# Performance work log

Measured on AMD Instinct MI355X. Metric: run time of the kernel, lower is better.

## Reference

```python
import jax, jax.numpy as jnp
import numpy as np

VAR0, VAR1 = 0.1, 0.2          # SSD encode variances
POS_T, NEG_T, NPR = 0.5, 0.4, 3  # pos/neg thresholds, negpos_ratio
BBOX_ALPHA, CONF_ALPHA = 1.5, 1.0


def point_form(b):
    # cxcywh -> x1y1x2y2
    return jnp.concatenate([b[..., :2] - b[..., 2:] / 2, b[..., :2] + b[..., 2:] / 2], -1)


def jaccard(a, b):
    # a:[n,4], b:[m,4] in xyxy -> IoU [n,m]
    tl = jnp.maximum(a[:, None, :2], b[None, :, :2])
    br = jnp.minimum(a[:, None, 2:], b[None, :, 2:])
    inter = jnp.prod(jnp.clip(br - tl, 0.0), -1)
    area_a = jnp.prod(a[:, 2:] - a[:, :2], -1)[:, None]
    area_b = jnp.prod(b[:, 2:] - b[:, :2], -1)[None, :]
    return inter / jnp.clip(area_a + area_b - inter, 1e-10)


def encode(matched, priors):
    # matched: xyxy GT per prior; priors: cxcywh
    g_c = ((matched[:, :2] + matched[:, 2:]) / 2 - priors[:, :2]) / (VAR0 * priors[:, 2:])
    g_wh = jnp.log(jnp.clip((matched[:, 2:] - matched[:, :2]) / priors[:, 2:], 1e-8)) / VAR1
    return jnp.concatenate([g_c, g_wh], -1)


def match_one(gt_box, gt_lab, priors):
    # gt_box:[G,4] xyxy, gt_lab:[G], priors:[P,4] cxcywh
    ov = jaccard(gt_box, point_form(priors))            # [G,P]
    bt_over = ov.max(0)                                  # best GT overlap per prior [P]
    bt_idx = ov.argmax(0)                                # [P]
    bp_idx = ov.argmax(1)                                # best prior per GT [G]
    G = gt_box.shape[0]
    bt_over = bt_over.at[bp_idx].set(2.0)                # force-match best priors
    bt_idx = bt_idx.at[bp_idx].set(jnp.arange(G))
    matched = gt_box[bt_idx]                             # [P,4]
    conf_t = gt_lab[bt_idx]
    conf_t = jnp.where(bt_over < POS_T, jnp.where(bt_over < NEG_T, 0, -1), conf_t)
    return encode(matched, priors), conf_t


def reference(loc_data, conf_data, priors, gt_bboxes, gt_labels):
    B, P, C = conf_data.shape
    loc_t, conf_t = jax.vmap(match_one)(gt_bboxes, gt_labels, priors)
    loc_t = jax.lax.stop_gradient(loc_t)                 # targets are detached in torch
    pos = conf_t > 0                                     # [B,P]
    num_pos = pos.sum(-1)                                # [B]
    dt = loc_data.dtype
    pos_w = pos.astype(dt) / jnp.clip(num_pos, 1).astype(dt)[:, None]

    # localization: per-image-normalized smooth L1 over positives
    d = loc_data - loc_t
    sl1 = jnp.where(jnp.abs(d) < 1.0, 0.5 * d * d, jnp.abs(d) - 0.5)
    loss_B = (pos_w[:, :, None] * sl1).sum() * BBOX_ALPHA

    # OHEM confidence loss: mine top negpos_ratio*num_pos hardest negatives per image
    loss_c = jax.nn.logsumexp(conf_data, -1) - conf_data[..., 0]
    loss_c = jnp.where(pos | (conf_t < 0), 0.0, jax.lax.stop_gradient(loss_c))
    rank = jnp.argsort(jnp.argsort(-loss_c, -1), -1)     # descending rank [B,P]
    num_neg = jnp.clip(NPR * num_pos, 0, P - 1)
    neg = (rank < num_neg[:, None]) & (conf_t == 0)
    keep = (pos | neg).astype(dt)
    logp = jax.nn.log_softmax(conf_data, -1)
    tgt = jnp.clip(conf_t, 0)
    ce = -jnp.take_along_axis(logp, tgt[..., None], -1)[..., 0]
    loss_C = (keep * ce).sum() * CONF_ALPHA

    return jnp.stack([loss_B, loss_C]) / B               # [2]: (loss_B, loss_C)


def setup_inputs() -> dict:
    key = jax.random.key(0)
    k = jax.random.split(key, 8)
    B, P, C, G = 16, 19248, 81, 16
    loc_data = jax.random.normal(k[0], (B, P, 4), jnp.float32)
    conf_data = jax.random.normal(k[1], (B, P, C), jnp.float32)
    pc = jax.random.uniform(k[2], (B, P, 2)) * 0.9 + 0.05
    pwh = jax.random.uniform(k[3], (B, P, 2)) * 0.25 + 0.05
    priors = jnp.concatenate([pc, pwh], -1).astype(jnp.float32)  # cxcywh
    gc = jax.random.uniform(k[4], (B, G, 2)) * 0.8 + 0.1
    gwh = jax.random.uniform(k[5], (B, G, 2)) * 0.3 + 0.05
    gt_bboxes = jnp.clip(point_form(jnp.concatenate([gc, gwh], -1)), 0.0, 1.0).astype(jnp.float32)
    gt_labels = jax.random.randint(k[6], (B, G), 1, C)
    return {"loc_data": loc_data, "conf_data": conf_data, "priors": priors,
            "gt_bboxes": gt_bboxes, "gt_labels": gt_labels}
```

## Files before the change

kernel.cpp:

```cpp
#include <hip/hip_runtime.h>
#include <math.h>

#define NB 16
#define NP 19248
#define NC 81
#define NG 16
#define NBC 301
#define NWPB (NBC * 4)

static __device__ __forceinline__ float smoothl1(float d) {
    float a = fabsf(d);
    return (a < 1.f) ? 0.5f * d * d : (a - 0.5f);
}

static __device__ __forceinline__ unsigned long long umax64(unsigned long long a, unsigned long long b) {
    return a > b ? a : b;
}

__global__ void __launch_bounds__(256, 6) k_main(
        const float* __restrict__ conf,
        const float* __restrict__ loc,
        const float* __restrict__ priors,
        const float* __restrict__ gtb,
        const int* __restrict__ gtl,
        unsigned long long* __restrict__ kws,
        float* __restrict__ mlc,
        int* __restrict__ pnp, float* __restrict__ psl, float* __restrict__ pce,
        float* __restrict__ out) {
    __shared__ float sc[4][1296];
    const int b = blockIdx.y;
    const int tid = threadIdx.x;
    if (b == 0 && blockIdx.x == 0 && tid < 2) out[tid] = 0.f;
    const int w = tid >> 6, lane = tid & 63;
    const int rb = blockIdx.x * 64 + w * 16;
    const bool wvalid = rb < NP;
    const int rb_c = wvalid ? rb : (NP - 16);

    const float4* src = (const float4*)(conf + ((size_t)b * NP + rb_c) * 81);
    float4* dst = (float4*)sc[w];
    #pragma unroll
    for (int i = 0; i < 5; ++i) dst[lane + 64 * i] = src[lane + 64 * i];
    if (lane < 4) dst[lane + 320] = src[lane + 320];

    const int r = lane >> 2, c = lane & 3;
    const int p = rb_c + r;
    const int bp = b * NP + p;
    const int wslot = blockIdx.x * 4 + w;

    const float4 prr = *(const float4*)(priors + (size_t)bp * 4);
    const float px1 = prr.x - prr.z * 0.5f, py1 = prr.y - prr.w * 0.5f;
    const float px2 = prr.x + prr.z * 0.5f, py2 = prr.y + prr.w * 0.5f;
    const float areaP = (px2 - px1) * (py2 - py1);
    const unsigned int pk = 0xFFFFFFFFu - (unsigned int)p;
    unsigned long long kq = 0ULL;
    #pragma unroll
    for (int j = 0; j < 4; ++j) {
        const int g = c * 4 + j;
        const float4 gb = *(const float4*)(gtb + (size_t)(b * NG + g) * 4);
        float iw = fminf(gb.z, px2) - fmaxf(gb.x, px1);
        float ih = fminf(gb.w, py2) - fmaxf(gb.y, py1);
        float inter = fmaxf(iw, 0.f) * fmaxf(ih, 0.f);
        float areaG = (gb.z - gb.x) * (gb.w - gb.y);
        float ov = inter / fmaxf(areaG + areaP - inter, 1e-10f);
        const unsigned long long ub = (unsigned long long)__float_as_uint(ov) << 32;
        kq = umax64(kq, ub | (unsigned long long)(15 - g));
        unsigned long long kg = ub | (unsigned long long)pk;
        #pragma unroll
        for (int off = 4; off <= 32; off <<= 1)
            kg = umax64(kg, (unsigned long long)__shfl_xor((unsigned long long)kg, off));
        if (lane < 4)
            kws[((size_t)(b * NG) + lane * 4 + j) * NWPB + wslot] = kg;
    }
    kq = umax64(kq, (unsigned long long)__shfl_xor((unsigned long long)kq, 1, 4));
    kq = umax64(kq, (unsigned long long)__shfl_xor((unsigned long long)kq, 2, 4));
    const float over = __uint_as_float((unsigned int)(kq >> 32));
    const int bi = 15 - (int)(kq & 0xFULL);

    int ct;
    if (over < 0.4f) ct = 0;
    else if (over < 0.5f) ct = -1;
    else ct = gtl[b * NG + bi];
    if (!wvalid) ct = 0;
    const int tgt = ct > 0 ? ct : 0;

    __builtin_amdgcn_wave_barrier();

    const float* row = sc[w] + r * 81;
    float s = 0.f, ctg = 0.f;
    #pragma unroll
    for (int k = 0; k < 21; ++k) {
        int cc = c + 4 * k;
        if (cc < 81) {
            float v = row[cc];
            s += __expf(v);
            ctg += (cc == tgt) ? v : 0.f;
        }
    }
    s += __shfl_xor(s, 1, 4);   s += __shfl_xor(s, 2, 4);
    ctg += __shfl_xor(ctg, 1, 4); ctg += __shfl_xor(ctg, 2, 4);
    const float c0 = row[0];
    const float lse = __logf(s);

    if (c == 0 && wvalid) mlc[bp] = (ct == 0) ? (lse - c0) : -1.0f;

    float vsl = 0.f, vce = 0.f; int vnp = 0;
    if (c == 0 && ct > 0) {
        const float4 gb = *(const float4*)(gtb + (size_t)(b * NG + bi) * 4);
        float lt0 = ((gb.x + gb.z) * 0.5f - prr.x) / (0.1f * prr.z);
        float lt1 = ((gb.y + gb.w) * 0.5f - prr.y) / (0.1f * prr.w);
        float lt2 = logf(fmaxf((gb.z - gb.x) / prr.z, 1e-8f)) / 0.2f;
        float lt3 = logf(fmaxf((gb.w - gb.y) / prr.w, 1e-8f)) / 0.2f;
        const float4 l4 = *(const float4*)(loc + (size_t)bp * 4);
        vsl = smoothl1(l4.x - lt0) + smoothl1(l4.y - lt1) +
              smoothl1(l4.z - lt2) + smoothl1(l4.w - lt3);
        vce = lse - ctg;
        vnp = 1;
    }
    #pragma unroll
    for (int o = 32; o >= 1; o >>= 1) {
        vnp += __shfl_xor(vnp, o);
        vsl += __shfl_xor(vsl, o);
        vce += __shfl_xor(vce, o);
    }
    if (lane == 0) {
        const int idx = b * NWPB + wslot;
        pnp[idx] = vnp; psl[idx] = vsl; pce[idx] = vce;
    }
}

__global__ void __launch_bounds__(1024) k_finish(
        const float* __restrict__ conf,
        const float* __restrict__ loc,
        const float* __restrict__ priors,
        const float* __restrict__ gtb,
        const int* __restrict__ gtl,
        const unsigned long long* __restrict__ kws,
        const float* __restrict__ mlc,
        const int* __restrict__ pnp,
        const float* __restrict__ psl,
        const float* __restrict__ pce,
        float* __restrict__ out) {
    const int b = blockIdx.x, tid = threadIdx.x;
    __shared__ unsigned int hist[4096];
    __shared__ unsigned long long list[1024];
    __shared__ unsigned int s_jstar, s_need, s_cnt;
    __shared__ unsigned long long s_thr;
    __shared__ unsigned int wtot[16], wsuf[16];
    __shared__ float wsum[16];
    __shared__ int wnp[16]; __shared__ float wsl[16], wcp[16];
    __shared__ int s_np; __shared__ float s_sl, s_cp;
    __shared__ unsigned int fprior[16];
    __shared__ unsigned int zap[16];
    __shared__ int s_dnp; __shared__ float s_dsl, s_dce;

    const float4* v4 = (const float4*)(mlc + (size_t)b * NP);
    float4 rv[5];
    #pragma unroll
    for (int j = 0; j < 5; ++j) {
        int i = tid + 1024 * j;
        rv[j] = (i < NP / 4) ? v4[i] : make_float4(-1.f, -1.f, -1.f, -1.f);
    }

    {
        int np_ = 0; float sl_ = 0.f, cp_ = 0.f;
        for (int i = tid; i < NWPB; i += 1024) {
            np_ += pnp[b * NWPB + i];
            sl_ += psl[b * NWPB + i];
            cp_ += pce[b * NWPB + i];
        }
        #pragma unroll
        for (int o = 32; o >= 1; o >>= 1) {
            np_ += __shfl_xor(np_, o);
            sl_ += __shfl_xor(sl_, o);
            cp_ += __shfl_xor(cp_, o);
        }
        if ((tid & 63) == 0) { wnp[tid >> 6] = np_; wsl[tid >> 6] = sl_; wcp[tid >> 6] = cp_; }
    }
    {
        const int wv = tid >> 6, lane = tid & 63;
        unsigned long long kk = 0ULL;
        const unsigned long long* kp = kws + ((size_t)(b * NG) + wv) * NWPB;
        for (int i = lane; i < NWPB; i += 64) kk = umax64(kk, kp[i]);
        #pragma unroll
        for (int o = 32; o >= 1; o >>= 1)
            kk = umax64(kk, (unsigned long long)__shfl_xor((unsigned long long)kk, o));
        if (lane == 0) fprior[wv] = 0xFFFFFFFFu - (unsigned int)(kk & 0xFFFFFFFFULL);
    }
    if (tid == 0) { s_cnt = 0u; s_thr = ~0ULL; s_dnp = 0; s_dsl = 0.f; s_dce = 0.f; }
    for (int i = tid; i < 4096; i += 1024) hist[i] = 0u;
    __syncthreads();

    if (tid < 64) {
        const int g = tid >> 2, c = tid & 3;
        const unsigned int pstar = fprior[g];
        bool winner = true;
        for (int g2 = g + 1; g2 < NG; ++g2) if (fprior[g2] == pstar) winner = false;
        int old_ct = 1;
        if (winner) {
            const int pp = (int)pstar;
            const int bpp = b * NP + pp;
            const float4 prr = *(const float4*)(priors + (size_t)bpp * 4);
            const float px1 = prr.x - prr.z * 0.5f, py1 = prr.y - prr.w * 0.5f;
            const float px2 = prr.x + prr.z * 0.5f, py2 = prr.y + prr.w * 0.5f;
            const float areaP = (px2 - px1) * (py2 - py1);
            unsigned long long kq = 0ULL;
            #pragma unroll
            for (int j = 0; j < 4; ++j) {
                const int g2 = c * 4 + j;
                const float4 gb = *(const float4*)(gtb + (size_t)(b * NG + g2) * 4);
                float iw = fminf(gb.z, px2) - fmaxf(gb.x, px1);
                float ih = fminf(gb.w, py2) - fmaxf(gb.y, py1);
                float inter = fmaxf(iw, 0.f) * fmaxf(ih, 0.f);
                float areaG = (gb.z - gb.x) * (gb.w - gb.y);
                float ov = inter / fmaxf(areaG + areaP - inter, 1e-10f);
                kq = umax64(kq, ((unsigned long long)__float_as_uint(ov) << 32) |
                                (unsigned long long)(15 - g2));
            }
            kq = umax64(kq, (unsigned long long)__shfl_xor((unsigned long long)kq, 1, 4));
            kq = umax64(kq, (unsigned long long)__shfl_xor((unsigned long long)kq, 2, 4));
            const float over = __uint_as_float((unsigned int)(kq >> 32));
            const int obi = 15 - (int)(kq & 0xFULL);
            if (over < 0.4f) old_ct = 0;
            else if (over < 0.5f) old_ct = -1;
            else old_ct = gtl[b * NG + obi];
            const int new_lab = gtl[b * NG + g];
            const int old_tgt = old_ct > 0 ? old_ct : 0;
            const float* row = conf + (size_t)bpp * 81;
            float s = 0.f, vnew = 0.f, vold = 0.f;
            #pragma unroll
            for (int k = 0; k < 21; ++k) {
                int cc = c + 4 * k;
                if (cc < 81) {
                    float v = row[cc];
                    s += __expf(v);
                    vnew += (cc == new_lab) ? v : 0.f;
                    vold += (cc == old_tgt) ? v : 0.f;
                }
            }
            s += __shfl_xor(s, 1, 4);       s += __shfl_xor(s, 2, 4);
            vnew += __shfl_xor(vnew, 1, 4); vnew += __shfl_xor(vnew, 2, 4);
            vold += __shfl_xor(vold, 1, 4); vold += __shfl_xor(vold, 2, 4);
            if (c == 0) {
                const float lse = __logf(s);
                float dce = (old_ct > 0) ? (vold - vnew) : (lse - vnew);
                const float4 gb = *(const float4*)(gtb + (size_t)(b * NG + g) * 4);
                float lt0 = ((gb.x + gb.z) * 0.5f - prr.x) / (0.1f * prr.z);
                float lt1 = ((gb.y + gb.w) * 0.5f - prr.y) / (0.1f * prr.w);
                float lt2 = logf(fmaxf((gb.z - gb.x) / prr.z, 1e-8f)) / 0.2f;
                float lt3 = logf(fmaxf((gb.w - gb.y) / prr.w, 1e-8f)) / 0.2f;
                const float4 l4 = *(const float4*)(loc + (size_t)bpp * 4);
                float dsl = smoothl1(l4.x - lt0) + smoothl1(l4.y - lt1) +
                            smoothl1(l4.z - lt2) + smoothl1(l4.w - lt3);
                if (old_ct > 0) {
                    const float4 go = *(const float4*)(gtb + (size_t)(b * NG + obi) * 4);
                    float ot0 = ((go.x + go.z) * 0.5f - prr.x) / (0.1f * prr.z);
                    float ot1 = ((go.y + go.w) * 0.5f - prr.y) / (0.1f * prr.w);
                    float ot2 = logf(fmaxf((go.z - go.x) / prr.z, 1e-8f)) / 0.2f;
                    float ot3 = logf(fmaxf((go.w - go.y) / prr.w, 1e-8f)) / 0.2f;
                    dsl -= smoothl1(l4.x - ot0) + smoothl1(l4.y - ot1) +
                           smoothl1(l4.z - ot2) + smoothl1(l4.w - ot3);
                }
                if (old_ct <= 0) atomicAdd(&s_dnp, 1);
                atomicAdd(&s_dsl, dsl);
                atomicAdd(&s_dce, dce);
            }
        }
        if (c == 0) zap[g] = (winner && old_ct == 0) ? pstar : 0xFFFFFFFFu;
    }
    __syncthreads();

    #pragma unroll
    for (int z = 0; z < NG; ++z) {
        unsigned int u = zap[z];
        if (u != 0xFFFFFFFFu) {
            unsigned int q = u >> 2, cc = u & 3u;
            if ((int)(q & 1023u) == tid) {
                unsigned int jj = q >> 10;
                #pragma unroll
                for (int j = 0; j < 5; ++j) if ((unsigned int)j == jj) {
                    if (cc == 0) rv[j].x = -1.f;
                    else if (cc == 1) rv[j].y = -1.f;
                    else if (cc == 2) rv[j].z = -1.f;
                    else rv[j].w = -1.f;
                }
            }
        }
    }
    if (tid == 0) {
        int np_ = s_dnp; float sl_ = s_dsl, cp_ = s_dce;
        #pragma unroll
        for (int i = 0; i < 16; ++i) { np_ += wnp[i]; sl_ += wsl[i]; cp_ += wcp[i]; }
        s_np = np_; s_sl = sl_; s_cp = cp_;
    }
    #pragma unroll
    for (int j = 0; j < 5; ++j) {
        float vv[4] = {rv[j].x, rv[j].y, rv[j].z, rv[j].w};
        #pragma unroll
        for (int cth = 0; cth < 4; ++cth)
            if (vv[cth] >= 0.f)
                atomicAdd(&hist[min((unsigned int)(vv[cth] * 256.f), 4095u)], 1u);
    }
    __syncthreads();
    const int np = s_np;
    const unsigned int k = (unsigned int)min(3 * np, NP - 1);

    if (k > 0) {
        unsigned int c0 = hist[tid * 4], c1 = hist[tid * 4 + 1],
                     c2 = hist[tid * 4 + 2], c3 = hist[tid * 4 + 3];
        unsigned int t2 = c2 + c3, t1 = c1 + t2, t0 = c0 + t1;
        unsigned int s = t0;
        const int lane = tid & 63, w = tid >> 6;
        #pragma unroll
        for (int o = 1; o < 64; o <<= 1) {
            unsigned int vv = __shfl_down(s, o);
            if (lane + o < 64) s += vv;
        }
        if (lane == 0) wtot[w] = s;
        __syncthreads();
        if (tid < 16) {
            unsigned int acc = 0;
            for (int j = tid + 1; j < 16; ++j) acc += wtot[j];
            wsuf[tid] = acc;
        }
        __syncthreads();
        const unsigned int base = wsuf[w] + (s - t0);
        unsigned int b0 = base + t0, b1 = base + t1, b2 = base + t2, b3 = base + c3;
        hist[tid * 4] = b0; hist[tid * 4 + 1] = b1;
        hist[tid * 4 + 2] = b2; hist[tid * 4 + 3] = b3;
        __syncthreads();
        const unsigned int total = hist[0];
        if (k >= total) {
            if (tid == 0) s_thr = 0ULL;
        } else {
            unsigned int n3 = (tid * 4 + 4 < 4096) ? hist[tid * 4 + 4] : 0u;
            if (b0 >= k && b1 < k) { s_jstar = tid * 4;     s_need = k - b1; }
            if (b1 >= k && b2 < k) { s_jstar = tid * 4 + 1; s_need = k - b2; }
            if (b2 >= k && b3 < k) { s_jstar = tid * 4 + 2; s_need = k - b3; }
            if (b3 >= k && n3 < k) { s_jstar = tid * 4 + 3; s_need = k - n3; }
            __syncthreads();
            const unsigned int jstar = s_jstar, need = s_need;
            #pragma unroll
            for (int j = 0; j < 5; ++j) {
                float vv[4] = {rv[j].x, rv[j].y, rv[j].z, rv[j].w};
                #pragma unroll
                for (int cth = 0; cth < 4; ++cth) {
                    if (vv[cth] >= 0.f &&
                        min((unsigned int)(vv[cth] * 256.f), 4095u) == jstar) {
                        unsigned int pos = atomicAdd(&s_cnt, 1u);
                        if (pos < 1024u) {
                            int pidx = 4 * (tid + 1024 * j) + cth;
                            list[pos] = ((unsigned long long)__float_as_uint(vv[cth]) << 32) |
                                        (unsigned long long)(0xFFFFFFFFu - (unsigned int)pidx);
                        }
                    }
                }
            }
            __syncthreads();
            const unsigned int cnt = s_cnt;
            if (cnt <= 1024u) {
                if (tid < (int)cnt) {
                    unsigned long long me = list[tid];
                    unsigned int rk = 0;
                    for (unsigned int j = 0; j < cnt; ++j) rk += (list[j] > me) ? 1u : 0u;
                    if (rk == need - 1) s_thr = me;
                }
            } else if (tid == 0) {
                s_thr = ((unsigned long long)__float_as_uint((float)jstar / 256.f)) << 32;
            }
        }
    }
    __syncthreads();
    const unsigned long long thr = s_thr;

    float sum = 0.f;
    #pragma unroll
    for (int j = 0; j < 5; ++j) {
        float vv[4] = {rv[j].x, rv[j].y, rv[j].z, rv[j].w};
        #pragma unroll
        for (int cth = 0; cth < 4; ++cth) {
            if (vv[cth] >= 0.f) {
                int pidx = 4 * (tid + 1024 * j) + cth;
                unsigned long long key = ((unsigned long long)__float_as_uint(vv[cth]) << 32) |
                                         (unsigned long long)(0xFFFFFFFFu - (unsigned int)pidx);
                if (key >= thr) sum += vv[cth];
            }
        }
    }
    #pragma unroll
    for (int o = 32; o >= 1; o >>= 1) sum += __shfl_xor(sum, o);
    if ((tid & 63) == 0) wsum[tid >> 6] = sum;
    __syncthreads();
    if (tid == 0) {
        float neg = 0.f;
        #pragma unroll
        for (int i = 0; i < 16; ++i) neg += wsum[i];
        float lb = s_sl / (float)max(np, 1);
        float lc = s_cp + neg;
        atomicAdd(&out[0], lb * 1.5f / (float)NB);
        atomicAdd(&out[1], lc / (float)NB);
    }
}

extern "C" void kernel_launch(void* const* d_in, const int* in_sizes, int n_in,
                              void* d_out, int out_size, void* d_ws, size_t ws_size,
                              hipStream_t stream) {
    const float* loc    = (const float*)d_in[0];
    const float* conf   = (const float*)d_in[1];
    const float* priors = (const float*)d_in[2];
    const float* gtb    = (const float*)d_in[3];
    const int*   gtl    = (const int*)d_in[4];
    float* out = (float*)d_out;

    char* w = (char*)d_ws;
    const size_t KWS = (size_t)NB * NG * NWPB * 8;
    const size_t P1  = (size_t)NB * NWPB * 4;
    unsigned long long* kws = (unsigned long long*)w;
    int*   pnp = (int*)  (w + KWS);
    float* psl = (float*)(w + KWS + P1);
    float* pce = (float*)(w + KWS + 2 * P1);
    float* mlc = (float*)(w + KWS + 3 * P1);

    k_main<<<dim3(NBC, NB), 256, 0, stream>>>(conf, loc, priors, gtb, gtl,
                                              kws, mlc, pnp, psl, pce, out);
    k_finish<<<NB, 1024, 0, stream>>>(conf, loc, priors, gtb, gtl,
                                      kws, mlc, pnp, psl, pce, out);
}
```

Before: 186.1 us.

## Fuse finish kernel into main kernel via last-block-per-image completion counter

Merges the two kernels into one. The last block to finish for each image, found with an atomic counter and thread fences, runs the matching fix-up, the histogram and the hard-negative top-k selection with 256 threads instead of a separate 1024-thread launch. A second counter lets the last image write the final outputs directly instead of using atomics, and a memset resets the counters each call. The aim is to remove a kernel launch and its gap and to overlap the per-image tail with other images still in progress. In exchange the tail runs with 4x fewer threads, rereads the mining values from global memory three times, and adds a memset launch.

```diff
diff --git a/kernel.cpp b/kernel.cpp
--- a/kernel.cpp
+++ b/kernel.cpp
@@ -7,6 +7,7 @@
 #define NG 16
 #define NBC 301
 #define NWPB (NBC * 4)
+#define NV4 (NP / 4)
 
 static __device__ __forceinline__ float smoothl1(float d) {
     float a = fabsf(d);
@@ -17,27 +18,29 @@
     return a > b ? a : b;
 }
 
-__global__ void __launch_bounds__(256, 6) k_main(
+__global__ void __launch_bounds__(256, 6) k_all(
         const float* __restrict__ conf,
         const float* __restrict__ loc,
         const float* __restrict__ priors,
         const float* __restrict__ gtb,
         const int* __restrict__ gtl,
+        unsigned int* __restrict__ cnt,
         unsigned long long* __restrict__ kws,
         float* __restrict__ mlc,
         int* __restrict__ pnp, float* __restrict__ psl, float* __restrict__ pce,
+        int* __restrict__ rnp, float* __restrict__ rsl, float* __restrict__ rlc,
         float* __restrict__ out) {
-    __shared__ float sc[4][1296];
+    __shared__ unsigned long long smem[3072];
+    float* sc = (float*)smem;
     const int b = blockIdx.y;
     const int tid = threadIdx.x;
-    if (b == 0 && blockIdx.x == 0 && tid < 2) out[tid] = 0.f;
     const int w = tid >> 6, lane = tid & 63;
     const int rb = blockIdx.x * 64 + w * 16;
     const bool wvalid = rb < NP;
     const int rb_c = wvalid ? rb : (NP - 16);
 
     const float4* src = (const float4*)(conf + ((size_t)b * NP + rb_c) * 81);
-    float4* dst = (float4*)sc[w];
+    float4* dst = (float4*)(sc + w * 1296);
     #pragma unroll
     for (int i = 0; i < 5; ++i) dst[lane + 64 * i] = src[lane + 64 * i];
     if (lane < 4) dst[lane + 320] = src[lane + 320];
@@ -85,7 +88,7 @@
 
     __builtin_amdgcn_wave_barrier();
 
-    const float* row = sc[w] + r * 81;
+    const float* row = sc + w * 1296 + r * 81;
     float s = 0.f, ctg = 0.f;
     #pragma unroll
     for (int k = 0; k < 21; ++k) {
@@ -126,44 +129,28 @@
         const int idx = b * NWPB + wslot;
         pnp[idx] = vnp; psl[idx] = vsl; pce[idx] = vce;
     }
-}
-
-__global__ void __launch_bounds__(1024) k_finish(
-        const float* __restrict__ conf,
-        const float* __restrict__ loc,
-        const float* __restrict__ priors,
-        const float* __restrict__ gtb,
-        const int* __restrict__ gtl,
-        const unsigned long long* __restrict__ kws,
-        const float* __restrict__ mlc,
-        const int* __restrict__ pnp,
-        const float* __restrict__ psl,
-        const float* __restrict__ pce,
-        float* __restrict__ out) {
-    const int b = blockIdx.x, tid = threadIdx.x;
-    __shared__ unsigned int hist[4096];
-    __shared__ unsigned long long list[1024];
-    __shared__ unsigned int s_jstar, s_need, s_cnt;
+
+    __shared__ int s_last;
+    __threadfence();
+    if (tid == 0) s_last = (atomicAdd(&cnt[b], 1u) == NBC - 1) ? 1 : 0;
+    __syncthreads();
+    if (!s_last) return;
+    __threadfence();
+
+    unsigned int* hist = (unsigned int*)smem;
+    unsigned long long* list = smem + 2048;
+    __shared__ unsigned int s_jstar, s_need, s_cnt, s_total;
     __shared__ unsigned long long s_thr;
-    __shared__ unsigned int wtot[16], wsuf[16];
-    __shared__ float wsum[16];
-    __shared__ int wnp[16]; __shared__ float wsl[16], wcp[16];
+    __shared__ int wnp4[4]; __shared__ float wsl4[4], wcp4[4];
+    __shared__ unsigned int wtot4[4], wsuf4[4];
+    __shared__ float wsum4[4];
     __shared__ int s_np; __shared__ float s_sl, s_cp;
-    __shared__ unsigned int fprior[16];
-    __shared__ unsigned int zap[16];
+    __shared__ unsigned int fprior[16], zap[16];
     __shared__ int s_dnp; __shared__ float s_dsl, s_dce;
-
-    const float4* v4 = (const float4*)(mlc + (size_t)b * NP);
-    float4 rv[5];
-    #pragma unroll
-    for (int j = 0; j < 5; ++j) {
-        int i = tid + 1024 * j;
-        rv[j] = (i < NP / 4) ? v4[i] : make_float4(-1.f, -1.f, -1.f, -1.f);
-    }
 
     {
         int np_ = 0; float sl_ = 0.f, cp_ = 0.f;
-        for (int i = tid; i < NWPB; i += 1024) {
+        for (int i = tid; i < NWPB; i += 256) {
             np_ += pnp[b * NWPB + i];
             sl_ += psl[b * NWPB + i];
             cp_ += pce[b * NWPB + i];
@@ -174,89 +161,88 @@
             sl_ += __shfl_xor(sl_, o);
             cp_ += __shfl_xor(cp_, o);
         }
-        if ((tid & 63) == 0) { wnp[tid >> 6] = np_; wsl[tid >> 6] = sl_; wcp[tid >> 6] = cp_; }
-    }
-    {
-        const int wv = tid >> 6, lane = tid & 63;
+        if (lane == 0) { wnp4[w] = np_; wsl4[w] = sl_; wcp4[w] = cp_; }
+    }
+    for (int q = 0; q < 4; ++q) {
+        const int g = w * 4 + q;
         unsigned long long kk = 0ULL;
-        const unsigned long long* kp = kws + ((size_t)(b * NG) + wv) * NWPB;
+        const unsigned long long* kp = kws + ((size_t)(b * NG) + g) * NWPB;
         for (int i = lane; i < NWPB; i += 64) kk = umax64(kk, kp[i]);
         #pragma unroll
         for (int o = 32; o >= 1; o >>= 1)
             kk = umax64(kk, (unsigned long long)__shfl_xor((unsigned long long)kk, o));
-        if (lane == 0) fprior[wv] = 0xFFFFFFFFu - (unsigned int)(kk & 0xFFFFFFFFULL);
+        if (lane == 0) fprior[g] = 0xFFFFFFFFu - (unsigned int)(kk & 0xFFFFFFFFULL);
     }
     if (tid == 0) { s_cnt = 0u; s_thr = ~0ULL; s_dnp = 0; s_dsl = 0.f; s_dce = 0.f; }
-    for (int i = tid; i < 4096; i += 1024) hist[i] = 0u;
     __syncthreads();
 
     if (tid < 64) {
-        const int g = tid >> 2, c = tid & 3;
-        const unsigned int pstar = fprior[g];
+        const int fg = tid >> 2, fc = tid & 3;
+        const unsigned int pstar = fprior[fg];
         bool winner = true;
-        for (int g2 = g + 1; g2 < NG; ++g2) if (fprior[g2] == pstar) winner = false;
+        for (int g2 = fg + 1; g2 < NG; ++g2) if (fprior[g2] == pstar) winner = false;
         int old_ct = 1;
         if (winner) {
             const int pp = (int)pstar;
             const int bpp = b * NP + pp;
-            const float4 prr = *(const float4*)(priors + (size_t)bpp * 4);
-            const float px1 = prr.x - prr.z * 0.5f, py1 = prr.y - prr.w * 0.5f;
-            const float px2 = prr.x + prr.z * 0.5f, py2 = prr.y + prr.w * 0.5f;
-            const float areaP = (px2 - px1) * (py2 - py1);
-            unsigned long long kq = 0ULL;
+            const float4 fpr = *(const float4*)(priors + (size_t)bpp * 4);
+            const float fx1 = fpr.x - fpr.z * 0.5f, fy1 = fpr.y - fpr.w * 0.5f;
+            const float fx2 = fpr.x + fpr.z * 0.5f, fy2 = fpr.y + fpr.w * 0.5f;
+            const float fareaP = (fx2 - fx1) * (fy2 - fy1);
+            unsigned long long kq2 = 0ULL;
             #pragma unroll
             for (int j = 0; j < 4; ++j) {
-                const int g2 = c * 4 + j;
+                const int g2 = fc * 4 + j;
                 const float4 gb = *(const float4*)(gtb + (size_t)(b * NG + g2) * 4);
-                float iw = fminf(gb.z, px2) - fmaxf(gb.x, px1);
-                float ih = fminf(gb.w, py2) - fmaxf(gb.y, py1);
+                float iw = fminf(gb.z, fx2) - fmaxf(gb.x, fx1);
+                float ih = fminf(gb.w, fy2) - fmaxf(gb.y, fy1);
                 float inter = fmaxf(iw, 0.f) * fmaxf(ih, 0.f);
                 float areaG = (gb.z - gb.x) * (gb.w - gb.y);
-                float ov = inter / fmaxf(areaG + areaP - inter, 1e-10f);
-                kq = umax64(kq, ((unsigned long long)__float_as_uint(ov) << 32) |
-                                (unsigned long long)(15 - g2));
-            }
-            kq = umax64(kq, (unsigned long long)__shfl_xor((unsigned long long)kq, 1, 4));
-            kq = umax64(kq, (unsigned long long)__shfl_xor((unsigned long long)kq, 2, 4));
-            const float over = __uint_as_float((unsigned int)(kq >> 32));
-            const int obi = 15 - (int)(kq & 0xFULL);
-            if (over < 0.4f) old_ct = 0;
-            else if (over < 0.5f) old_ct = -1;
+                float ov = inter / fmaxf(areaG + fareaP - inter, 1e-10f);
+                kq2 = umax64(kq2, ((unsigned long long)__float_as_uint(ov) << 32) |
+                                  (unsigned long long)(15 - g2));
+            }
+            kq2 = umax64(kq2, (unsigned long long)__shfl_xor((unsigned long long)kq2, 1, 4));
+            kq2 = umax64(kq2, (unsigned long long)__shfl_xor((unsigned long long)kq2, 2, 4));
+            const float fover = __uint_as_float((unsigned int)(kq2 >> 32));
+            const int obi = 15 - (int)(kq2 & 0xFULL);
+            if (fover < 0.4f) old_ct = 0;
+            else if (fover < 0.5f) old_ct = -1;
             else old_ct = gtl[b * NG + obi];
-            const int new_lab = gtl[b * NG + g];
+            const int new_lab = gtl[b * NG + fg];
             const int old_tgt = old_ct > 0 ? old_ct : 0;
-            const float* row = conf + (size_t)bpp * 81;
-            float s = 0.f, vnew = 0.f, vold = 0.f;
+            const float* frow = conf + (size_t)bpp * 81;
+            float fs = 0.f, vnew = 0.f, vold = 0.f;
             #pragma unroll
             for (int k = 0; k < 21; ++k) {
-                int cc = c + 4 * k;
+                int cc = fc + 4 * k;
                 if (cc < 81) {
-                    float v = row[cc];
-                    s += __expf(v);
+                    float v = frow[cc];
+                    fs += __expf(v);
                     vnew += (cc == new_lab) ? v : 0.f;
                     vold += (cc == old_tgt) ? v : 0.f;
                 }
             }
-            s += __shfl_xor(s, 1, 4);       s += __shfl_xor(s, 2, 4);
+            fs += __shfl_xor(fs, 1, 4);     fs += __shfl_xor(fs, 2, 4);
             vnew += __shfl_xor(vnew, 1, 4); vnew += __shfl_xor(vnew, 2, 4);
             vold += __shfl_xor(vold, 1, 4); vold += __shfl_xor(vold, 2, 4);
-            if (c == 0) {
-                const float lse = __logf(s);
-                float dce = (old_ct > 0) ? (vold - vnew) : (lse - vnew);
-                const float4 gb = *(const float4*)(gtb + (size_t)(b * NG + g) * 4);
-                float lt0 = ((gb.x + gb.z) * 0.5f - prr.x) / (0.1f * prr.z);
-                float lt1 = ((gb.y + gb.w) * 0.5f - prr.y) / (0.1f * prr.w);
-                float lt2 = logf(fmaxf((gb.z - gb.x) / prr.z, 1e-8f)) / 0.2f;
-                float lt3 = logf(fmaxf((gb.w - gb.y) / prr.w, 1e-8f)) / 0.2f;
+            if (fc == 0) {
+                const float flse = __logf(fs);
+                float dce = (old_ct > 0) ? (vold - vnew) : (flse - vnew);
+                const float4 gb = *(const float4*)(gtb + (size_t)(b * NG + fg) * 4);
+                float lt0 = ((gb.x + gb.z) * 0.5f - fpr.x) / (0.1f * fpr.z);
+                float lt1 = ((gb.y + gb.w) * 0.5f - fpr.y) / (0.1f * fpr.w);
+                float lt2 = logf(fmaxf((gb.z - gb.x) / fpr.z, 1e-8f)) / 0.2f;
+                float lt3 = logf(fmaxf((gb.w - gb.y) / fpr.w, 1e-8f)) / 0.2f;
                 const float4 l4 = *(const float4*)(loc + (size_t)bpp * 4);
                 float dsl = smoothl1(l4.x - lt0) + smoothl1(l4.y - lt1) +
                             smoothl1(l4.z - lt2) + smoothl1(l4.w - lt3);
                 if (old_ct > 0) {
                     const float4 go = *(const float4*)(gtb + (size_t)(b * NG + obi) * 4);
-                    float ot0 = ((go.x + go.z) * 0.5f - prr.x) / (0.1f * prr.z);
-                    float ot1 = ((go.y + go.w) * 0.5f - prr.y) / (0.1f * prr.w);
-                    float ot2 = logf(fmaxf((go.z - go.x) / prr.z, 1e-8f)) / 0.2f;
-                    float ot3 = logf(fmaxf((go.w - go.y) / prr.w, 1e-8f)) / 0.2f;
+                    float ot0 = ((go.x + go.z) * 0.5f - fpr.x) / (0.1f * fpr.z);
+                    float ot1 = ((go.y + go.w) * 0.5f - fpr.y) / (0.1f * fpr.w);
+                    float ot2 = logf(fmaxf((go.z - go.x) / fpr.z, 1e-8f)) / 0.2f;
+                    float ot3 = logf(fmaxf((go.w - go.y) / fpr.w, 1e-8f)) / 0.2f;
                     dsl -= smoothl1(l4.x - ot0) + smoothl1(l4.y - ot1) +
                            smoothl1(l4.z - ot2) + smoothl1(l4.w - ot3);
                 }
@@ -265,90 +251,77 @@
                 atomicAdd(&s_dce, dce);
             }
         }
-        if (c == 0) zap[g] = (winner && old_ct == 0) ? pstar : 0xFFFFFFFFu;
-    }
-    __syncthreads();
-
-    #pragma unroll
-    for (int z = 0; z < NG; ++z) {
-        unsigned int u = zap[z];
-        if (u != 0xFFFFFFFFu) {
-            unsigned int q = u >> 2, cc = u & 3u;
-            if ((int)(q & 1023u) == tid) {
-                unsigned int jj = q >> 10;
-                #pragma unroll
-                for (int j = 0; j < 5; ++j) if ((unsigned int)j == jj) {
-                    if (cc == 0) rv[j].x = -1.f;
-                    else if (cc == 1) rv[j].y = -1.f;
-                    else if (cc == 2) rv[j].z = -1.f;
-                    else rv[j].w = -1.f;
-                }
-            }
-        }
-    }
+        if (fc == 0) zap[fg] = (winner && old_ct == 0) ? pstar : 0xFFFFFFFFu;
+    }
+    __syncthreads();
+
+    if (tid < NG) {
+        unsigned int u = zap[tid];
+        if (u != 0xFFFFFFFFu) mlc[(size_t)b * NP + u] = -1.0f;
+    }
+    __threadfence_block();
     if (tid == 0) {
         int np_ = s_dnp; float sl_ = s_dsl, cp_ = s_dce;
         #pragma unroll
-        for (int i = 0; i < 16; ++i) { np_ += wnp[i]; sl_ += wsl[i]; cp_ += wcp[i]; }
+        for (int i = 0; i < 4; ++i) { np_ += wnp4[i]; sl_ += wsl4[i]; cp_ += wcp4[i]; }
         s_np = np_; s_sl = sl_; s_cp = cp_;
     }
-    #pragma unroll
-    for (int j = 0; j < 5; ++j) {
-        float vv[4] = {rv[j].x, rv[j].y, rv[j].z, rv[j].w};
-        #pragma unroll
-        for (int cth = 0; cth < 4; ++cth)
-            if (vv[cth] >= 0.f)
-                atomicAdd(&hist[min((unsigned int)(vv[cth] * 256.f), 4095u)], 1u);
+    for (int i = tid; i < 4096; i += 256) hist[i] = 0u;
+    __syncthreads();
+
+    const float4* mv4 = (const float4*)(mlc + (size_t)b * NP);
+    for (int i = tid; i < NV4; i += 256) {
+        float4 v = mv4[i];
+        if (v.x >= 0.f) atomicAdd(&hist[min((unsigned int)(v.x * 256.f), 4095u)], 1u);
+        if (v.y >= 0.f) atomicAdd(&hist[min((unsigned int)(v.y * 256.f), 4095u)], 1u);
+        if (v.z >= 0.f) atomicAdd(&hist[min((unsigned int)(v.z * 256.f), 4095u)], 1u);
+        if (v.w >= 0.f) atomicAdd(&hist[min((unsigned int)(v.w * 256.f), 4095u)], 1u);
     }
     __syncthreads();
     const int np = s_np;
     const unsigned int k = (unsigned int)min(3 * np, NP - 1);
 
     if (k > 0) {
-        unsigned int c0 = hist[tid * 4], c1 = hist[tid * 4 + 1],
-                     c2 = hist[tid * 4 + 2], c3 = hist[tid * 4 + 3];
-        unsigned int t2 = c2 + c3, t1 = c1 + t2, t0 = c0 + t1;
-        unsigned int s = t0;
-        const int lane = tid & 63, w = tid >> 6;
+        unsigned int ttot = 0;
+        for (int i = 0; i < 16; ++i) ttot += hist[tid * 16 + i];
+        unsigned int s2 = ttot;
         #pragma unroll
         for (int o = 1; o < 64; o <<= 1) {
-            unsigned int vv = __shfl_down(s, o);
-            if (lane + o < 64) s += vv;
-        }
-        if (lane == 0) wtot[w] = s;
+            unsigned int vv = __shfl_down(s2, o);
+            if (lane + o < 64) s2 += vv;
+        }
+        if (lane == 0) wtot4[w] = s2;
         __syncthreads();
-        if (tid < 16) {
-            unsigned int acc = 0;
-            for (int j = tid + 1; j < 16; ++j) acc += wtot[j];
-            wsuf[tid] = acc;
+        if (tid < 4) {
+            unsigned int a = 0;
+            for (int j = tid + 1; j < 4; ++j) a += wtot4[j];
+            wsuf4[tid] = a;
         }
         __syncthreads();
-        const unsigned int base = wsuf[w] + (s - t0);
-        unsigned int b0 = base + t0, b1 = base + t1, b2 = base + t2, b3 = base + c3;
-        hist[tid * 4] = b0; hist[tid * 4 + 1] = b1;
-        hist[tid * 4 + 2] = b2; hist[tid * 4 + 3] = b3;
+        const unsigned int base = wsuf4[w] + (s2 - ttot);
+        if (tid == 0) s_total = base + ttot;
+        unsigned int run = 0;
+        for (int i = 15; i >= 0; --i) {
+            unsigned int Sj1 = base + run;
+            run += hist[tid * 16 + i];
+            unsigned int Sj = base + run;
+            if (Sj >= k && Sj1 < k) { s_jstar = tid * 16 + i; s_need = k - Sj1; }
+        }
         __syncthreads();
-        const unsigned int total = hist[0];
-        if (k >= total) {
+        if (k >= s_total) {
             if (tid == 0) s_thr = 0ULL;
         } else {
-            unsigned int n3 = (tid * 4 + 4 < 4096) ? hist[tid * 4 + 4] : 0u;
-            if (b0 >= k && b1 < k) { s_jstar = tid * 4;     s_need = k - b1; }
-            if (b1 >= k && b2 < k) { s_jstar = tid * 4 + 1; s_need = k - b2; }
-            if (b2 >= k && b3 < k) { s_jstar = tid * 4 + 2; s_need = k - b3; }
-            if (b3 >= k && n3 < k) { s_jstar = tid * 4 + 3; s_need = k - n3; }
-            __syncthreads();
             const unsigned int jstar = s_jstar, need = s_need;
-            #pragma unroll
-            for (int j = 0; j < 5; ++j) {
-                float vv[4] = {rv[j].x, rv[j].y, rv[j].z, rv[j].w};
+            for (int i = tid; i < NV4; i += 256) {
+                float4 v = mv4[i];
+                float vv[4] = {v.x, v.y, v.z, v.w};
                 #pragma unroll
                 for (int cth = 0; cth < 4; ++cth) {
                     if (vv[cth] >= 0.f &&
                         min((unsigned int)(vv[cth] * 256.f), 4095u) == jstar) {
                         unsigned int pos = atomicAdd(&s_cnt, 1u);
                         if (pos < 1024u) {
-                            int pidx = 4 * (tid + 1024 * j) + cth;
+                            int pidx = 4 * i + cth;
                             list[pos] = ((unsigned long long)__float_as_uint(vv[cth]) << 32) |
                                         (unsigned long long)(0xFFFFFFFFu - (unsigned int)pidx);
                         }
@@ -356,12 +329,12 @@
                 }
             }
             __syncthreads();
-            const unsigned int cnt = s_cnt;
-            if (cnt <= 1024u) {
-                if (tid < (int)cnt) {
-                    unsigned long long me = list[tid];
+            const unsigned int cc2 = s_cnt;
+            if (cc2 <= 1024u) {
+                for (int e = tid; e < (int)cc2; e += 256) {
+                    unsigned long long me = list[e];
                     unsigned int rk = 0;
-                    for (unsigned int j = 0; j < cnt; ++j) rk += (list[j] > me) ? 1u : 0u;
+                    for (unsigned int j2 = 0; j2 < cc2; ++j2) rk += (list[j2] > me) ? 1u : 0u;
                     if (rk == need - 1) s_thr = me;
                 }
             } else if (tid == 0) {
@@ -373,13 +346,13 @@
     const unsigned long long thr = s_thr;
 
     float sum = 0.f;
-    #pragma unroll
-    for (int j = 0; j < 5; ++j) {
-        float vv[4] = {rv[j].x, rv[j].y, rv[j].z, rv[j].w};
+    for (int i = tid; i < NV4; i += 256) {
+        float4 v = mv4[i];
+        float vv[4] = {v.x, v.y, v.z, v.w};
         #pragma unroll
         for (int cth = 0; cth < 4; ++cth) {
             if (vv[cth] >= 0.f) {
-                int pidx = 4 * (tid + 1024 * j) + cth;
+                int pidx = 4 * i + cth;
                 unsigned long long key = ((unsigned long long)__float_as_uint(vv[cth]) << 32) |
                                          (unsigned long long)(0xFFFFFFFFu - (unsigned int)pidx);
                 if (key >= thr) sum += vv[cth];
@@ -388,16 +361,22 @@
     }
     #pragma unroll
     for (int o = 32; o >= 1; o >>= 1) sum += __shfl_xor(sum, o);
-    if ((tid & 63) == 0) wsum[tid >> 6] = sum;
+    if (lane == 0) wsum4[w] = sum;
     __syncthreads();
     if (tid == 0) {
-        float neg = 0.f;
-        #pragma unroll
-        for (int i = 0; i < 16; ++i) neg += wsum[i];
-        float lb = s_sl / (float)max(np, 1);
-        float lc = s_cp + neg;
-        atomicAdd(&out[0], lb * 1.5f / (float)NB);
-        atomicAdd(&out[1], lc / (float)NB);
+        float neg = wsum4[0] + wsum4[1] + wsum4[2] + wsum4[3];
+        rnp[b] = np; rsl[b] = s_sl; rlc[b] = s_cp + neg;
+        __threadfence();
+        if (atomicAdd(&cnt[NB], 1u) == NB - 1) {
+            __threadfence();
+            float lb = 0.f, lc = 0.f;
+            for (int i = 0; i < NB; ++i) {
+                lb += rsl[i] / (float)max(rnp[i], 1);
+                lc += rlc[i];
+            }
+            out[0] = lb * 1.5f / (float)NB;
+            out[1] = lc / (float)NB;
+        }
     }
 }
 
@@ -414,14 +393,18 @@
     char* w = (char*)d_ws;
     const size_t KWS = (size_t)NB * NG * NWPB * 8;
     const size_t P1  = (size_t)NB * NWPB * 4;
-    unsigned long long* kws = (unsigned long long*)w;
-    int*   pnp = (int*)  (w + KWS);
-    float* psl = (float*)(w + KWS + P1);
-    float* pce = (float*)(w + KWS + 2 * P1);
-    float* mlc = (float*)(w + KWS + 3 * P1);
-
-    k_main<<<dim3(NBC, NB), 256, 0, stream>>>(conf, loc, priors, gtb, gtl,
-                                              kws, mlc, pnp, psl, pce, out);
-    k_finish<<<NB, 1024, 0, stream>>>(conf, loc, priors, gtb, gtl,
-                                      kws, mlc, pnp, psl, pce, out);
+    unsigned int* cnt = (unsigned int*)w;
+    unsigned long long* kws = (unsigned long long*)(w + 128);
+    int*   pnp = (int*)  (w + 128 + KWS);
+    float* psl = (float*)(w + 128 + KWS + P1);
+    float* pce = (float*)(w + 128 + KWS + 2 * P1);
+    int*   rnp = (int*)  (w + 128 + KWS + 3 * P1);
+    float* rsl = (float*)(w + 128 + KWS + 3 * P1 + 64);
+    float* rlc = (float*)(w + 128 + KWS + 3 * P1 + 128);
+    float* mlc = (float*)(w + 128 + KWS + 3 * P1 + 192);
+
+    hipMemsetAsync(cnt, 0, 128, stream);
+    k_all<<<dim3(NBC, NB), 256, 0, stream>>>(conf, loc, priors, gtb, gtl,
+                                             cnt, kws, mlc, pnp, psl, pce,
+                                             rnp, rsl, rlc, out);
 }
```

After: 737.3 us. 3.96x slower.
